# Performance work log

Hardware: AMD Instinct MI355X
Metric: run time of the kernel (lower is better)

## Reference

```python
import jax, jax.numpy as jnp
import numpy as np

N, D, E = 16384, 256, 8
H = D // 2  # gate hidden


def setup_inputs() -> dict:
    key = jax.random.key(0)
    ks = jax.random.split(key, 10)
    s = lambda fan_in: 1.0 / np.sqrt(fan_in)
    return {
        "x":   jax.random.normal(ks[0], (N, D), dtype=jnp.float32),
        # gate: Linear(D, D//2) -> ReLU -> Linear(D//2, E) -> Softmax
        "Wg1": jax.random.uniform(ks[1], (D, H), jnp.float32, -s(D), s(D)),
        "bg1": jax.random.uniform(ks[2], (H,), jnp.float32, -s(D), s(D)),
        "Wg2": jax.random.uniform(ks[3], (H, E), jnp.float32, -s(H), s(H)),
        "bg2": jax.random.uniform(ks[4], (E,), jnp.float32, -s(H), s(H)),
        # experts: per-expert Linear(D,D) -> ReLU -> (Dropout eval=identity) -> Linear(D,D)
        "W1": jax.random.uniform(ks[5], (E, D, D), jnp.float32, -s(D), s(D)),
        "b1": jax.random.uniform(ks[6], (E, D), jnp.float32, -s(D), s(D)),
        "W2": jax.random.uniform(ks[7], (E, D, D), jnp.float32, -s(D), s(D)),
        "b2": jax.random.uniform(ks[8], (E, D), jnp.float32, -s(D), s(D)),
    }


def reference(x, Wg1, bg1, Wg2, bg2, W1, b1, W2, b2):
    # gate: [N, E] softmax over experts
    g = jax.nn.softmax(jax.nn.relu(x @ Wg1 + bg1) @ Wg2 + bg2, axis=-1)
    # all experts applied densely via batched GEMMs (fuses the Python loop)
    h = jax.nn.relu(jnp.einsum("nd,edh->neh", x, W1) + b1)  # [N, E, D]
    y = jnp.einsum("neh,ehd->ned", h, W2) + b2              # [N, E, D]
    # weighted combine: sum_e g[n,e] * y[n,e,:]
    return jnp.einsum("ned,ne->nd", y, g)
```

## Files before the change

kernel.cpp:

```cpp
#include <hip/hip_runtime.h>


typedef unsigned short USH;
typedef float f32x4 __attribute__((ext_vector_type(4)));
typedef __bf16 bf16x8 __attribute__((ext_vector_type(8)));

#define AS1 __attribute__((address_space(1)))
#define AS3 __attribute__((address_space(3)))

__device__ __forceinline__ USH f2bf(float f) {
  unsigned int u = __float_as_uint(f);
  u += 0x7fffu + ((u >> 16) & 1u);
  return (USH)(u >> 16);
}

__device__ __forceinline__ void gl2lds16(const void* g, void* l) {
  __builtin_amdgcn_global_load_lds((AS1 const void*)g, (AS3 void*)l, 16, 0, 0);
}


__global__ __launch_bounds__(256) void k_prep(
    const float* __restrict__ x,
    const float* __restrict__ Wg1,
    const float* __restrict__ W1,
    const float* __restrict__ W2,
    USH* __restrict__ xb, USH* __restrict__ wg1t,
    USH* __restrict__ w1t, USH* __restrict__ w2t) {
  __shared__ float T[64][65];
  int b = blockIdx.x, tid = threadIdx.x;

  if (b < 2048) {
    size_t i8 = ((size_t)b * 256 + tid) * 8;
    float4 a = *(const float4*)(x + i8);
    float4 c = *(const float4*)(x + i8 + 4);
    USH v[8];
    v[0] = f2bf(a.x); v[1] = f2bf(a.y); v[2] = f2bf(a.z); v[3] = f2bf(a.w);
    v[4] = f2bf(c.x); v[5] = f2bf(c.y); v[6] = f2bf(c.z); v[7] = f2bf(c.w);
    *(uint4*)(xb + i8) = *(const uint4*)v;
  } else if (b < 2176) {
    int bp = b - 2048;
    int e = bp >> 4, tl = bp & 15;
    int c0 = (tl >> 2) * 64, h0 = (tl & 3) * 64;
    const float* src = W1 + (size_t)e * 65536;
#pragma unroll
    for (int p = 0; p < 4; ++p) {
      int r = p * 16 + (tid >> 4), d4 = (tid & 15) * 4;
      float4 v = *(const float4*)(src + (size_t)(c0 + r) * 256 + h0 + d4);
      T[r][d4] = v.x; T[r][d4 + 1] = v.y; T[r][d4 + 2] = v.z; T[r][d4 + 3] = v.w;
    }
    __syncthreads();
#pragma unroll
    for (int p = 0; p < 4; ++p) {
      int hr = p * 16 + (tid >> 4), c4 = (tid & 15) * 4;
      USH w[4];
#pragma unroll
      for (int j = 0; j < 4; ++j) w[j] = f2bf(T[c4 + j][hr]);
      *(uint2*)(w1t + (size_t)e * 65536 + (size_t)(h0 + hr) * 256 + c0 + c4) = *(const uint2*)w;
    }
  } else if (b < 2184) {
    int bp = b - 2176;
    int c0 = (bp >> 1) * 64, h0 = (bp & 1) * 64;
#pragma unroll
    for (int p = 0; p < 4; ++p) {
      int r = p * 16 + (tid >> 4), d4 = (tid & 15) * 4;
      float4 v = *(const float4*)(Wg1 + (size_t)(c0 + r) * 128 + h0 + d4);
      T[r][d4] = v.x; T[r][d4 + 1] = v.y; T[r][d4 + 2] = v.z; T[r][d4 + 3] = v.w;
    }
    __syncthreads();
#pragma unroll
    for (int p = 0; p < 4; ++p) {
      int hr = p * 16 + (tid >> 4), c4 = (tid & 15) * 4;
      USH w[4];
#pragma unroll
      for (int j = 0; j < 4; ++j) w[j] = f2bf(T[c4 + j][hr]);
      *(uint2*)(wg1t + (size_t)(h0 + hr) * 256 + c0 + c4) = *(const uint2*)w;
    }
  } else {
    int bp = b - 2184;
    int e = bp >> 4, tl = bp & 15;
    int h0 = (tl >> 2) * 64, d0 = (tl & 3) * 64;
    const float* src = W2 + (size_t)e * 65536;
#pragma unroll
    for (int p = 0; p < 4; ++p) {
      int r = p * 16 + (tid >> 4), d4 = (tid & 15) * 4;
      float4 v = *(const float4*)(src + (size_t)(h0 + r) * 256 + d0 + d4);
      T[r][d4] = v.x; T[r][d4 + 1] = v.y; T[r][d4 + 2] = v.z; T[r][d4 + 3] = v.w;
    }
    __syncthreads();
#pragma unroll
    for (int p = 0; p < 4; ++p) {
      int dr = p * 16 + (tid >> 4), h4 = (tid & 15) * 4;
      USH w[4];
#pragma unroll
      for (int j = 0; j < 4; ++j) w[j] = f2bf(T[h4 + j][dr]);
      *(uint2*)(w2t + (size_t)(d0 + dr) * 2048 + e * 256 + h0 + h4) = *(const uint2*)w;
    }
  }
}


__global__ __launch_bounds__(256) void k_gate(const USH* __restrict__ xb,
                                              const USH* __restrict__ wg1t,
                                              const float* __restrict__ bg1,
                                              const float* __restrict__ wg2,
                                              const float* __restrict__ bg2,
                                              float* __restrict__ g) {
  __shared__ __align__(16) USH As[32 * 64];
  __shared__ __align__(16) USH Bs[128 * 64];
  __shared__ float hg[32 * 129];
  __shared__ float bg1s[128];
  __shared__ float w2s[128 * 8];
  __shared__ float b2s[8];
  __shared__ float lg[32 * 8];

  int tid = threadIdx.x;
  int wave = tid >> 6, lane = tid & 63;
  int quad = lane >> 4, l16 = lane & 15;
  int sw = l16 & 7;
  int wr = wave >> 1, wc = wave & 1;
  int rowBase = blockIdx.x * 32;

  for (int t = tid; t < 1024; t += 256) w2s[t] = wg2[t];
  if (tid < 8) b2s[tid] = bg2[tid];
  if (tid < 128) bg1s[tid] = bg1[tid];

  f32x4 acc[4] = {};
  for (int kt = 0; kt < 4; ++kt) {
    int kb = kt * 64;
    {
      int r = tid >> 3, c8 = (tid & 7) ^ (r & 7);
      gl2lds16(xb + (size_t)(rowBase + r) * 256 + kb + c8 * 8, As + (size_t)tid * 8);
    }
#pragma unroll
    for (int c = 0; c < 4; ++c) {
      int i = c * 256 + tid;
      int r = i >> 3, c8 = (i & 7) ^ (r & 7);
      gl2lds16(wg1t + (size_t)r * 256 + kb + c8 * 8, Bs + (size_t)i * 8);
    }
    __syncthreads();
#pragma unroll
    for (int kkc = 0; kkc < 8; kkc += 4) {
      bf16x8 av = *(const bf16x8*)(As + (wr * 16 + l16) * 64 + (((kkc + quad) ^ sw) * 8));
#pragma unroll
      for (int j = 0; j < 4; ++j) {
        bf16x8 bv = *(const bf16x8*)(Bs + (wc * 64 + j * 16 + l16) * 64 + (((kkc + quad) ^ sw) * 8));
        acc[j] = __builtin_amdgcn_mfma_f32_16x16x32_bf16(av, bv, acc[j], 0, 0, 0);
      }
    }
    __syncthreads();
  }

#pragma unroll
  for (int j = 0; j < 4; ++j)
#pragma unroll
    for (int r = 0; r < 4; ++r) {
      int row = wr * 16 + quad * 4 + r;
      int col = wc * 64 + j * 16 + l16;
      hg[row * 129 + col] = fmaxf(acc[j][r] + bg1s[col], 0.0f);
    }
  __syncthreads();

  {
    int row = tid >> 3, p = tid & 7;
    float s = b2s[p];
    for (int k = 0; k < 128; ++k) s += hg[row * 129 + k] * w2s[k * 8 + p];
    lg[row * 8 + p] = s;
  }
  __syncthreads();

  if (tid < 32) {
    float l[8];
    float m = -1e30f;
#pragma unroll
    for (int e = 0; e < 8; ++e) { l[e] = lg[tid * 8 + e]; m = fmaxf(m, l[e]); }
    float s = 0.0f;
#pragma unroll
    for (int e = 0; e < 8; ++e) { l[e] = expf(l[e] - m); s += l[e]; }
    float inv = 1.0f / s;
    size_t grow = rowBase + tid;
#pragma unroll
    for (int e = 0; e < 8; ++e) g[grow * 8 + e] = l[e] * inv;
  }
}


__global__ __launch_bounds__(512) void k_moe(const USH* __restrict__ xb,
                                             const USH* __restrict__ w1t,
                                             const USH* __restrict__ w2t,
                                             const float* __restrict__ b1,
                                             const float* __restrict__ b2,
                                             const float* __restrict__ g,
                                             float* __restrict__ out) {
  __shared__ __align__(16) USH xs[4 * 64 * 64];
  __shared__ __align__(16) USH Hs[64 * 256];
  __shared__ __align__(16) USH Ws[2][256 * 64];
  __shared__ float b1s[256];
  __shared__ float b2s[2048];
  __shared__ float gs[512];

  int tid = threadIdx.x;
  int wave = tid >> 6, lane = tid & 63;
  int quad = lane >> 4, l16 = lane & 15;
  int sw = l16 & 7;
  int rowBase = blockIdx.x * 64;

#pragma unroll
  for (int it = 0; it < 4; ++it) {
    int i = it * 512 + tid;
    int kt = i >> 9, rem = i & 511;
    int r = rem >> 3, slot = rem & 7;
    int c8 = slot ^ (r & 7);
    gl2lds16(xb + (size_t)(rowBase + r) * 256 + kt * 64 + c8 * 8, xs + (size_t)i * 8);
  }
#pragma unroll
  for (int t = tid; t < 2048; t += 512) b2s[t] = b2[t];
  gs[tid] = g[(size_t)rowBase * 8 + tid];

  auto STAGE = [&](int T, int bf) {
    int e = T >> 3;
    int cb = (T & 3) * 64;
    const USH* src;
    size_t stride;
    if (T & 4) { src = w2t + e * 256 + cb;               stride = 2048; }
    else       { src = w1t + (size_t)e * 65536 + cb;     stride = 256;  }
    USH* dst = &Ws[bf][0];
#pragma unroll
    for (int it = 0; it < 4; ++it) {
      int i = it * 512 + tid;
      int r = i >> 3, slot = i & 7;
      int c8 = slot ^ (r & 7);
      gl2lds16(src + (size_t)r * stride + c8 * 8, dst + (size_t)i * 8);
    }
  };

  int wh = wave >> 1, wn = wave & 1;
  int wn2 = wave >> 2, wd = wave & 3;

  f32x4 oacc[2][4] = {};
  int buf = 0;
  STAGE(0, 0);

#pragma unroll 1
  for (int e = 0; e < 8; ++e) {
    f32x4 hacc[4][2] = {};
    if (tid < 256) b1s[tid] = b1[e * 256 + tid];

    for (int kt = 0; kt < 4; ++kt) {
      __syncthreads();
      int T = e * 8 + kt;
      if (T < 63) STAGE(T + 1, buf ^ 1);
      const USH* W = &Ws[buf][0];
#pragma unroll
      for (int kkc = 0; kkc < 8; kkc += 4) {
        int cs = ((kkc + quad) ^ sw) * 8;
        bf16x8 av[4], bv[2];
#pragma unroll
        for (int i = 0; i < 4; ++i)
          av[i] = *(const bf16x8*)(W + (wh * 64 + i * 16 + l16) * 64 + cs);
#pragma unroll
        for (int j = 0; j < 2; ++j)
          bv[j] = *(const bf16x8*)(xs + kt * 4096 + (wn * 32 + j * 16 + l16) * 64 + cs);
#pragma unroll
        for (int i = 0; i < 4; ++i)
#pragma unroll
          for (int j = 0; j < 2; ++j)
            hacc[i][j] = __builtin_amdgcn_mfma_f32_16x16x32_bf16(av[i], bv[j], hacc[i][j], 0, 0, 0);
      }
      buf ^= 1;
    }

#pragma unroll
    for (int i = 0; i < 4; ++i) {
      int c8 = i * 2 + (quad >> 1);
      int hb = wh * 64 + i * 16 + quad * 4;
#pragma unroll
      for (int j = 0; j < 2; ++j) {
        int n = wn * 32 + j * 16 + l16;
        float gg = gs[n * 8 + e];
        USH w4[4];
#pragma unroll
        for (int r = 0; r < 4; ++r)
          w4[r] = f2bf(fmaxf(hacc[i][j][r] + b1s[hb + r], 0.0f) * gg);
        int off = n * 256 + wh * 64 + (c8 ^ (n & 7)) * 8 + (quad & 1) * 4;
        *(uint2*)(Hs + off) = *(const uint2*)w4;
      }
    }

    for (int ht = 0; ht < 4; ++ht) {
      __syncthreads();
      int T = e * 8 + 4 + ht;
      if (T < 63) STAGE(T + 1, buf ^ 1);
      const USH* W = &Ws[buf][0];
#pragma unroll
      for (int kkc = 0; kkc < 8; kkc += 4) {
        int cs = ((kkc + quad) ^ sw) * 8;
        bf16x8 av[2], bv[4];
#pragma unroll
        for (int i = 0; i < 2; ++i)
          av[i] = *(const bf16x8*)(Hs + (wn2 * 32 + i * 16 + l16) * 256 + ht * 64 + cs);
#pragma unroll
        for (int j = 0; j < 4; ++j)
          bv[j] = *(const bf16x8*)(W + (wd * 64 + j * 16 + l16) * 64 + cs);
#pragma unroll
        for (int i = 0; i < 2; ++i)
#pragma unroll
          for (int j = 0; j < 4; ++j)
            oacc[i][j] = __builtin_amdgcn_mfma_f32_16x16x32_bf16(av[i], bv[j], oacc[i][j], 0, 0, 0);
      }
      buf ^= 1;
    }
  }

#pragma unroll
  for (int i = 0; i < 2; ++i)
#pragma unroll
    for (int r = 0; r < 4; ++r) {
      int n = wn2 * 32 + i * 16 + quad * 4 + r;
      const float* gr = gs + n * 8;
      size_t grow = (size_t)(rowBase + n) * 256;
#pragma unroll
      for (int j = 0; j < 4; ++j) {
        int d = wd * 64 + j * 16 + l16;
        float bias = 0.0f;
#pragma unroll
        for (int ee = 0; ee < 8; ++ee) bias += gr[ee] * b2s[ee * 256 + d];
        out[grow + d] = oacc[i][j][r] + bias;
      }
    }
}


extern "C" void kernel_launch(void* const* d_in, const int* in_sizes, int n_in,
                              void* d_out, int out_size, void* d_ws, size_t ws_size,
                              hipStream_t stream) {
  const float* x   = (const float*)d_in[0];
  const float* Wg1 = (const float*)d_in[1];
  const float* bg1 = (const float*)d_in[2];
  const float* Wg2 = (const float*)d_in[3];
  const float* bg2 = (const float*)d_in[4];
  const float* W1  = (const float*)d_in[5];
  const float* b1  = (const float*)d_in[6];
  const float* W2  = (const float*)d_in[7];
  const float* b2  = (const float*)d_in[8];
  float* out = (float*)d_out;

  char* ws = (char*)d_ws;
  USH*   xb   = (USH*)(ws);
  USH*   w1t  = (USH*)(ws + 8388608);
  USH*   wg1t = (USH*)(ws + 9437184);
  USH*   w2t  = (USH*)(ws + 9502720);
  float* g    = (float*)(ws + 10584064);

  hipLaunchKernelGGL(k_prep, dim3(2312), dim3(256), 0, stream,
                     x, Wg1, W1, W2, xb, wg1t, w1t, w2t);
  hipLaunchKernelGGL(k_gate, dim3(512), dim3(256), 0, stream,
                     xb, wg1t, bg1, Wg2, bg2, g);
  hipLaunchKernelGGL(k_moe, dim3(256), dim3(512), 0, stream,
                     xb, w1t, w2t, b1, b2, g, out);
}
```

Measured before the change: 149.2 us.

## Triple-buffer weight tiles with prefetch depth two and keep x in registers

Switches the weight staging from a double buffer to a triple buffer, prefetching two chunks ahead. Each chunk now waits with a partial s_waitcnt vmcnt(4) plus a raw s_barrier instead of a full __syncthreads. The x tile is loaded once into registers and its LDS region is reused as the third weight buffer. All b1 biases are preloaded up front, and MFMA sections get a raised s_setprio. The goal is to hide global-to-LDS latency and cut barrier and LDS-read overhead, at the cost of more registers and hand-tuned waitcnt logic that relies on in-order vmcnt accounting, including a wrap-around prefetch of extra tiles.

Result: slower. 164.4 us (+10.2%).

```diff
diff --git a/kernel.cpp b/kernel.cpp
--- a/kernel.cpp
+++ b/kernel.cpp
@@ -17,6 +17,12 @@
 __device__ __forceinline__ void gl2lds16(const void* g, void* l) {
   __builtin_amdgcn_global_load_lds((AS1 const void*)g, (AS3 void*)l, 16, 0, 0);
 }
+
+#define CHUNK_SYNC() do { \
+  __builtin_amdgcn_sched_barrier(0); \
+  asm volatile("s_waitcnt vmcnt(4) lgkmcnt(0)" ::: "memory"); \
+  __builtin_amdgcn_s_barrier(); \
+  __builtin_amdgcn_sched_barrier(0); } while (0)
 
 
 __global__ __launch_bounds__(256) void k_prep(
@@ -191,10 +197,9 @@
                                              const float* __restrict__ b2,
                                              const float* __restrict__ g,
                                              float* __restrict__ out) {
-  __shared__ __align__(16) USH xs[4 * 64 * 64];
+  __shared__ __align__(16) USH Ws[3][256 * 64];
   __shared__ __align__(16) USH Hs[64 * 256];
-  __shared__ __align__(16) USH Ws[2][256 * 64];
-  __shared__ float b1s[256];
+  __shared__ float b1s[2048];
   __shared__ float b2s[2048];
   __shared__ float gs[512];
 
@@ -210,63 +215,80 @@
     int kt = i >> 9, rem = i & 511;
     int r = rem >> 3, slot = rem & 7;
     int c8 = slot ^ (r & 7);
-    gl2lds16(xb + (size_t)(rowBase + r) * 256 + kt * 64 + c8 * 8, xs + (size_t)i * 8);
-  }
-#pragma unroll
-  for (int t = tid; t < 2048; t += 512) b2s[t] = b2[t];
+    gl2lds16(xb + (size_t)(rowBase + r) * 256 + kt * 64 + c8 * 8, &Ws[2][0] + (size_t)i * 8);
+  }
+#pragma unroll
+  for (int t = 0; t < 4; ++t) {
+    b1s[t * 512 + tid] = b1[t * 512 + tid];
+    b2s[t * 512 + tid] = b2[t * 512 + tid];
+  }
   gs[tid] = g[(size_t)rowBase * 8 + tid];
 
-  auto STAGE = [&](int T, int bf) {
-    int e = T >> 3;
-    int cb = (T & 3) * 64;
-    const USH* src;
+  __builtin_amdgcn_sched_barrier(0);
+  asm volatile("s_waitcnt vmcnt(0) lgkmcnt(0)" ::: "memory");
+  __builtin_amdgcn_s_barrier();
+  __builtin_amdgcn_sched_barrier(0);
+
+  auto STAGE = [&](int src, int bf) {
+    int e = src >> 3;
+    int cbo = (src & 3) * 64;
+    const USH* sp;
     size_t stride;
-    if (T & 4) { src = w2t + e * 256 + cb;               stride = 2048; }
-    else       { src = w1t + (size_t)e * 65536 + cb;     stride = 256;  }
+    if (src & 4) { sp = w2t + e * 256 + cbo;           stride = 2048; }
+    else         { sp = w1t + (size_t)e * 65536 + cbo; stride = 256;  }
     USH* dst = &Ws[bf][0];
 #pragma unroll
     for (int it = 0; it < 4; ++it) {
       int i = it * 512 + tid;
       int r = i >> 3, slot = i & 7;
       int c8 = slot ^ (r & 7);
-      gl2lds16(src + (size_t)r * stride + c8 * 8, dst + (size_t)i * 8);
+      gl2lds16(sp + (size_t)r * stride + c8 * 8, dst + (size_t)i * 8);
     }
   };
 
   int wh = wave >> 1, wn = wave & 1;
   int wn2 = wave >> 2, wd = wave & 3;
 
+  STAGE(0, 0);
+  STAGE(1, 1);
+
+  bf16x8 xr[4][2][2];
+#pragma unroll
+  for (int kt = 0; kt < 4; ++kt)
+#pragma unroll
+    for (int c = 0; c < 2; ++c)
+#pragma unroll
+      for (int j = 0; j < 2; ++j)
+        xr[kt][c][j] = *(const bf16x8*)(&Ws[2][0] + kt * 4096 +
+                         (wn * 32 + j * 16 + l16) * 64 + (((c * 4 + quad) ^ sw) * 8));
+
   f32x4 oacc[2][4] = {};
-  int buf = 0;
-  STAGE(0, 0);
 
 #pragma unroll 1
   for (int e = 0; e < 8; ++e) {
     f32x4 hacc[4][2] = {};
-    if (tid < 256) b1s[tid] = b1[e * 256 + tid];
-
+
+#pragma unroll
     for (int kt = 0; kt < 4; ++kt) {
-      __syncthreads();
       int T = e * 8 + kt;
-      if (T < 63) STAGE(T + 1, buf ^ 1);
-      const USH* W = &Ws[buf][0];
-#pragma unroll
-      for (int kkc = 0; kkc < 8; kkc += 4) {
-        int cs = ((kkc + quad) ^ sw) * 8;
-        bf16x8 av[4], bv[2];
+      CHUNK_SYNC();
+      STAGE((T + 2) & 63, (T + 2) % 3);
+      const USH* W = &Ws[T % 3][0];
+      __builtin_amdgcn_s_setprio(1);
+#pragma unroll
+      for (int c = 0; c < 2; ++c) {
+        int cs = ((c * 4 + quad) ^ sw) * 8;
+        bf16x8 av[4];
 #pragma unroll
         for (int i = 0; i < 4; ++i)
           av[i] = *(const bf16x8*)(W + (wh * 64 + i * 16 + l16) * 64 + cs);
 #pragma unroll
-        for (int j = 0; j < 2; ++j)
-          bv[j] = *(const bf16x8*)(xs + kt * 4096 + (wn * 32 + j * 16 + l16) * 64 + cs);
-#pragma unroll
         for (int i = 0; i < 4; ++i)
 #pragma unroll
           for (int j = 0; j < 2; ++j)
-            hacc[i][j] = __builtin_amdgcn_mfma_f32_16x16x32_bf16(av[i], bv[j], hacc[i][j], 0, 0, 0);
-      }
-      buf ^= 1;
+            hacc[i][j] = __builtin_amdgcn_mfma_f32_16x16x32_bf16(av[i], xr[kt][c][j], hacc[i][j], 0, 0, 0);
+      }
+      __builtin_amdgcn_s_setprio(0);
     }
 
 #pragma unroll
@@ -280,20 +302,22 @@
         USH w4[4];
 #pragma unroll
         for (int r = 0; r < 4; ++r)
-          w4[r] = f2bf(fmaxf(hacc[i][j][r] + b1s[hb + r], 0.0f) * gg);
+          w4[r] = f2bf(fmaxf(hacc[i][j][r] + b1s[e * 256 + hb + r], 0.0f) * gg);
         int off = n * 256 + wh * 64 + (c8 ^ (n & 7)) * 8 + (quad & 1) * 4;
         *(uint2*)(Hs + off) = *(const uint2*)w4;
       }
     }
 
+#pragma unroll
     for (int ht = 0; ht < 4; ++ht) {
-      __syncthreads();
       int T = e * 8 + 4 + ht;
-      if (T < 63) STAGE(T + 1, buf ^ 1);
-      const USH* W = &Ws[buf][0];
-#pragma unroll
-      for (int kkc = 0; kkc < 8; kkc += 4) {
-        int cs = ((kkc + quad) ^ sw) * 8;
+      CHUNK_SYNC();
+      STAGE((T + 2) & 63, (T + 2) % 3);
+      const USH* W = &Ws[T % 3][0];
+      __builtin_amdgcn_s_setprio(1);
+#pragma unroll
+      for (int c = 0; c < 2; ++c) {
+        int cs = ((c * 4 + quad) ^ sw) * 8;
         bf16x8 av[2], bv[4];
 #pragma unroll
         for (int i = 0; i < 2; ++i)
@@ -307,9 +331,11 @@
           for (int j = 0; j < 4; ++j)
             oacc[i][j] = __builtin_amdgcn_mfma_f32_16x16x32_bf16(av[i], bv[j], oacc[i][j], 0, 0, 0);
       }
-      buf ^= 1;
-    }
-  }
+      __builtin_amdgcn_s_setprio(0);
+    }
+  }
+
+  asm volatile("s_waitcnt vmcnt(0)" ::: "memory");
 
 #pragma unroll
   for (int i = 0; i < 2; ++i)
```
